# Kernel optimization log

Measured on AMD Instinct MI355X. Metric: run time of the kernel, lower is better.

Reference implementation:

```python
import jax, jax.numpy as jnp
import numpy as np

N_NODES = 30000
N_EDGES = 480000
N0, N1 = 64, 16            # hidden irreps: 64x0e (scalars) + 16x1o (vectors)
NUM_LAYERS = 3
NUM_ATOM_TYPES = 100
ATOM_EMB = 64
BOND_DIM, RAD_DIM = 8, 8   # edge_attr_dim=16 -> dim//2 bonded, (dim+1)//2 radial
MAX_RADIUS = 5.0
DEG_NORM = 1.0 / (16.0 ** 0.5)   # 1/sqrt(avg degree), NequIP-style aggregation norm


def soft_one_hot(d, number=RAD_DIM):
    # e3nn soft_one_hot_linspace, basis='gaussian', cutoff=True
    values = jnp.linspace(0.0, MAX_RADIUS, number + 2)[1:-1]
    step = MAX_RADIUS / (number + 1)
    diff = (d[:, None] - values) / step
    return jnp.exp(-diff ** 2) / 1.12


def setup_inputs() -> dict:
    key = jax.random.key(0)
    ks = jax.random.split(key, 16)
    pos = jax.random.normal(ks[0], (N_NODES, 3), jnp.float32) * 2.0
    edge_index = jax.random.randint(ks[1], (2, N_EDGES), 0, N_NODES)
    bond_mask = jax.random.randint(ks[2], (N_EDGES,), 0, 2)
    atom_type = jax.random.randint(ks[3], (N_NODES,), 0, NUM_ATOM_TYPES)

    def p(k, shape, scale):
        return jax.random.normal(k, shape, jnp.float32) * scale

    W_TP = N0 + N1 + N0 + 2 * N1   # per-edge tensor-product path weights (176)
    atom_emb = p(ks[4], (NUM_ATOM_TYPES, ATOM_EMB), 1.0)
    bond_emb = p(ks[5], (2, BOND_DIM), 1.0)
    w_init = p(ks[6], (ATOM_EMB, N0), ATOM_EMB ** -0.5)
    mlp_w1 = p(ks[7], (NUM_LAYERS, BOND_DIM + RAD_DIM, 64), 16 ** -0.5)
    mlp_b1 = jnp.zeros((NUM_LAYERS, 64), jnp.float32)
    mlp_w2 = p(ks[8], (NUM_LAYERS, 64, W_TP), 64 ** -0.5)
    lin_s = p(ks[9], (NUM_LAYERS, N0 + N1, N0), (N0 + N1) ** -0.5)
    lin_v = p(ks[10], (NUM_LAYERS, N0 + 2 * N1, N1), (N0 + 2 * N1) ** -0.5)
    gate_w = p(ks[11], (NUM_LAYERS, N0, N1), N0 ** -0.5)
    hs1 = p(ks[12], (N0, N0), N0 ** -0.5)
    hg = p(ks[13], (N0, N1), N0 ** -0.5)
    hs2 = p(ks[14], (N0, 1), N0 ** -0.5)
    hv2 = p(ks[15], (N1, 1), N1 ** -0.5)
    return dict(pos=pos, edge_index=edge_index, bond_mask=bond_mask,
                atom_type=atom_type, atom_emb=atom_emb, bond_emb=bond_emb,
                w_init=w_init, mlp_w1=mlp_w1, mlp_b1=mlp_b1, mlp_w2=mlp_w2,
                lin_s=lin_s, lin_v=lin_v, gate_w=gate_w,
                hs1=hs1, hg=hg, hs2=hs2, hv2=hv2)


def reference(pos, edge_index, bond_mask, atom_type, atom_emb, bond_emb,
              w_init, mlp_w1, mlp_b1, mlp_w2, lin_s, lin_v, gate_w,
              hs1, hg, hs2, hv2):
    n = pos.shape[0]
    src, dst = edge_index[0], edge_index[1]
    edge_vec = pos[src] - pos[dst]                       # [E,3] irregular gather
    r = jnp.linalg.norm(edge_vec, axis=-1)               # [E]
    u = edge_vec / jnp.maximum(r, 1e-9)[:, None]
    # Spherical harmonics lmax=1, 'component' normalization: Y0=1, Y1=sqrt(3)*r_hat
    y1 = (3.0 ** 0.5) * u                                # [E,3]
    edge_attr = jnp.concatenate([bond_emb[bond_mask], soft_one_hot(r)], axis=-1)  # [E,16]

    s = atom_emb[atom_type] @ w_init                     # [N,N0]; initial_linear (0e only)
    v = jnp.zeros((n, N1, 3), pos.dtype)                 # [N,N1,3]; 1o starts at zero

    for l in range(NUM_LAYERS):
        # radial/edge MLP -> per-edge tensor-product path weights
        w = jax.nn.silu(edge_attr @ mlp_w1[l] + mlp_b1[l]) @ mlp_w2[l]   # [E,176]
        w_ss, w_vs, w_sv, w_vv, w_cx = jnp.split(
            w, [N0, N0 + N1, 2 * N0 + N1, 2 * N0 + 2 * N1], axis=-1)
        se, ve = s[src], v[src]
        # CG tensor-product paths (Y0==1 absorbed):
        #   0e x 0e -> 0e (w_ss), 1o x 1o -> 0e dot (w_vs),
        #   0e x 1o -> 1o (w_sv), 1o x 0e -> 1o (w_vv), 1o x 1o -> 1e~cross (w_cx)
        m_s = jnp.concatenate(
            [w_ss * se, w_vs * jnp.einsum('eic,ec->ei', ve, y1)], axis=-1)  # [E,N0+N1]
        m_v = jnp.concatenate([
            w_sv[:, :, None] * se[:, :, None] * y1[:, None, :],
            w_vv[:, :, None] * ve,
            w_cx[:, :, None] * jnp.cross(ve, y1[:, None, :]),
        ], axis=1)                                       # [E,N0+2*N1,3]
        agg_s = jax.ops.segment_sum(m_s, dst, num_segments=n) * DEG_NORM
        agg_v = jax.ops.segment_sum(m_v, dst, num_segments=n) * DEG_NORM
        out_s = agg_s @ lin_s[l]                         # irrep-wise Linear, 0e
        out_v = jnp.einsum('nic,io->noc', agg_v, lin_v[l])  # irrep-wise Linear, 1o
        # gated nonlinearity + residual self-connection
        s = s + jax.nn.silu(out_s)
        v = v + out_v * jax.nn.sigmoid(out_s @ gate_w[l])[:, :, None]

    # EquivariantMLP output head -> 1x0e + 1x1o per node
    h = jax.nn.silu(s @ hs1)                             # [N,N0]
    vg = v * jax.nn.sigmoid(h @ hg)[:, :, None]          # gated vectors
    pred_s = h @ hs2                                     # [N,1]
    pred_v = jnp.einsum('nic,io->noc', vg, hv2)[:, 0, :] # [N,3]
    return jnp.concatenate([pred_s, pred_v], axis=-1)    # [N,4]
```

## Files before the change

kernel.cpp:

```cpp
#include <hip/hip_runtime.h>
#include <math.h>

#define N_NODES 30000
#define N_EDGES 480000
#define DEGN 0.25f
#define NBLK 1875
#define TPITCH 52

#define FENCE() do { asm volatile("" ::: "memory"); __builtin_amdgcn_sched_barrier(0); } while(0)

typedef __attribute__((ext_vector_type(8))) short short8;
typedef __attribute__((ext_vector_type(4))) float f32x4;

__device__ __forceinline__ float fsilu(float x){ return x / (1.f + __expf(-x)); }
__device__ __forceinline__ float fsig (float x){ return 1.f / (1.f + __expf(-x)); }

__device__ __forceinline__ unsigned bf16rn(float x){
  unsigned u = __float_as_uint(x);
  return (u + 0x7fffu + ((u>>16)&1u)) >> 16;
}
__device__ __forceinline__ unsigned pack2(float a, float b){
  return bf16rn(a) | (bf16rn(b)<<16);
}
__device__ __forceinline__ float bflo(unsigned u){ return __uint_as_float(u<<16); }
__device__ __forceinline__ float bfhi(unsigned u){ return __uint_as_float(u & 0xffff0000u); }

__global__ __launch_bounds__(256) void count2(const int* __restrict__ ei,
                                              int* __restrict__ deg_src,
                                              int* __restrict__ deg_dst)
{
  int e = blockIdx.x*256 + threadIdx.x;
  if (e >= N_EDGES) return;
  atomicAdd(deg_src + ei[e], 1);
  atomicAdd(deg_dst + ei[N_EDGES + e], 1);
}

__global__ __launch_bounds__(1024) void scan_deg2(
    const int* __restrict__ deg_src, int* __restrict__ off_src, int* __restrict__ cur_src,
    const int* __restrict__ deg_dst, int* __restrict__ off_dst, int* __restrict__ cur_dst)
{
  const int* deg = blockIdx.x ? deg_dst : deg_src;
  int* off = blockIdx.x ? off_dst : off_src;
  int* cur = blockIdx.x ? cur_dst : cur_src;
  __shared__ int part[1024];
  int t = threadIdx.x;
  int base = t*30;
  int local[30];
  int s = 0;
  #pragma unroll
  for (int i=0;i<30;i++){
    int idx = base + i;
    int d = (idx < N_NODES) ? deg[idx] : 0;
    local[i] = s; s += d;
  }
  part[t] = s; __syncthreads();
  for (int stp=1; stp<1024; stp<<=1){
    int v = (t >= stp) ? part[t-stp] : 0;
    __syncthreads();
    part[t] += v;
    __syncthreads();
  }
  int prefix = (t==0) ? 0 : part[t-1];
  #pragma unroll
  for (int i=0;i<30;i++){
    int idx = base + i;
    if (idx < N_NODES){ int o = prefix + local[i]; off[idx] = o; cur[idx] = o; }
  }
  if (t == 1023) off[N_NODES] = part[1023];
}

__global__ __launch_bounds__(256) void scatter_src(const int* __restrict__ ei,
                                                   int* __restrict__ cur,
                                                   int* __restrict__ csr_src,
                                                   int* __restrict__ pos_src)
{
  int e = blockIdx.x*256 + threadIdx.x;
  if (e >= N_EDGES) return;
  int p = atomicAdd(cur + ei[e], 1);
  csr_src[p] = e;
  pos_src[e] = p;
}

__global__ __launch_bounds__(256) void scatter_dst(const int* __restrict__ ei,
                                                   const int* __restrict__ pos_src,
                                                   int* __restrict__ cur,
                                                   int* __restrict__ gidx)
{
  int e = blockIdx.x*256 + threadIdx.x;
  if (e >= N_EDGES) return;
  int p = atomicAdd(cur + ei[N_EDGES + e], 1);
  gidx[p] = pos_src[e];
}

__global__ __launch_bounds__(256) void prep_edges2(
    const float* __restrict__ pos, const int* __restrict__ ei,
    const int* __restrict__ bond_mask, const float* __restrict__ bond_emb,
    const int* __restrict__ csr_src, uint4* __restrict__ rec)
{
  int k = blockIdx.x*256 + threadIdx.x;
  if (k >= N_EDGES) return;
  int e = csr_src[k];
  int src = ei[e], dst = ei[N_EDGES + e];
  float ax = pos[src*3+0], ay = pos[src*3+1], az = pos[src*3+2];
  float bx = pos[dst*3+0], by = pos[dst*3+1], bz = pos[dst*3+2];
  float vx = ax-bx, vy = ay-by, vz = az-bz;
  float r = sqrtf(vx*vx + vy*vy + vz*vz);
  float inv = 1.f / fmaxf(r, 1e-9f);
  const float s3 = 1.7320508075688772f;
  float yx = s3*vx*inv, yy = s3*vy*inv, yz = s3*vz*inv;
  int bm = bond_mask[e];
  float eav[16];
  #pragma unroll
  for (int q=0;q<8;q++) eav[q] = bond_emb[bm*8+q];
  const float step = 5.0f/9.0f;
  #pragma unroll
  for (int j=0;j<8;j++){
    float vj = (float)(j+1)*step;
    float d = (r - vj)/step;
    eav[8+j] = __expf(-d*d) * (1.0f/1.12f);
  }
  uint4 r0, r1, r2;
  r0.x = pack2(eav[0],eav[1]);  r0.y = pack2(eav[2],eav[3]);
  r0.z = pack2(eav[4],eav[5]);  r0.w = pack2(eav[6],eav[7]);
  r1.x = pack2(eav[8],eav[9]);  r1.y = pack2(eav[10],eav[11]);
  r1.z = pack2(eav[12],eav[13]);r1.w = pack2(eav[14],eav[15]);
  r2.x = __float_as_uint(yx); r2.y = __float_as_uint(yy);
  r2.z = __float_as_uint(yz); r2.w = (unsigned)src;
  rec[(size_t)k*3+0] = r0;
  rec[(size_t)k*3+1] = r1;
  rec[(size_t)k*3+2] = r2;
}

__global__ void prep_weights(const float* __restrict__ w2,
                             unsigned short* __restrict__ w2hi,
                             unsigned short* __restrict__ w2lo)
{
  int i = blockIdx.x*256 + threadIdx.x;
  if (i >= 3*176*64) return;
  int l = i / (176*64); int rem = i - l*(176*64);
  int n = rem / 64, k = rem - n*64;
  float w = w2[(size_t)l*64*176 + (size_t)k*176 + n];
  unsigned hi = bf16rn(w);
  float lo = w - __uint_as_float(hi<<16);
  w2hi[i] = (unsigned short)hi;
  w2lo[i] = (unsigned short)bf16rn(lo);
}

__global__ __launch_bounds__(256) void init_nodes(
    const int* __restrict__ atom_type, const float* __restrict__ atom_emb,
    const float* __restrict__ w_init, float* __restrict__ s)
{
  int n = blockIdx.x*256 + threadIdx.x;
  if (n >= N_NODES) return;
  int t = atom_type[n];
  float acc[64];
  #pragma unroll
  for (int o=0;o<64;o++) acc[o]=0.f;
  for (int k=0;k<64;k++){
    float ek = atom_emb[t*64+k];
    #pragma unroll
    for (int o=0;o<64;o++) acc[o] = fmaf(ek, w_init[k*64+o], acc[o]);
  }
  float4* so = (float4*)(s + (size_t)n*64);
  #pragma unroll
  for (int q=0;q<16;q++) so[q] = make_float4(acc[4*q],acc[4*q+1],acc[4*q+2],acc[4*q+3]);
}

__device__ __forceinline__ void mfma_tile(
    const unsigned short* __restrict__ W2hi, const unsigned short* __restrict__ W2lo,
    int colbase, const short8 (&bfr)[4][2], int wv, int l, unsigned char* tb)
{
  const unsigned short* ap = W2hi + (size_t)(colbase+(l&15))*64 + ((l>>4)*8);
  const unsigned short* aq = W2lo + (size_t)(colbase+(l&15))*64 + ((l>>4)*8);
  short8 ah0 = *(const short8*)ap;
  short8 ah1 = *(const short8*)(ap+32);
  short8 al0 = *(const short8*)aq;
  short8 al1 = *(const short8*)(aq+32);
  #pragma unroll
  for (int ntg=0;ntg<4;ntg++){
    f32x4 acc = {0.f,0.f,0.f,0.f};
    acc = __builtin_amdgcn_mfma_f32_16x16x32_bf16(ah0, bfr[ntg][0], acc, 0,0,0);
    acc = __builtin_amdgcn_mfma_f32_16x16x32_bf16(ah1, bfr[ntg][1], acc, 0,0,0);
    acc = __builtin_amdgcn_mfma_f32_16x16x32_bf16(al0, bfr[ntg][0], acc, 0,0,0);
    acc = __builtin_amdgcn_mfma_f32_16x16x32_bf16(al1, bfr[ntg][1], acc, 0,0,0);
    int e = wv*64 + ntg*16 + (l&15);
    uint2 pk; pk.x = pack2(acc[0],acc[1]); pk.y = pack2(acc[2],acc[3]);
    *(uint2*)(tb + (size_t)e*TPITCH + ((l>>4)*8)) = pk;
  }
}

__device__ __forceinline__ void decode_w(const unsigned char* tb, int t, float* w)
{
  const unsigned char* wr = tb + (size_t)t*TPITCH;
  uint4 c0 = *(const uint4*)wr;
  uint4 c1 = *(const uint4*)(wr+16);
  w[0]=bflo(c0.x); w[1]=bfhi(c0.x); w[2]=bflo(c0.y); w[3]=bfhi(c0.y);
  w[4]=bflo(c0.z); w[5]=bfhi(c0.z); w[6]=bflo(c0.w); w[7]=bfhi(c0.w);
  w[8]=bflo(c1.x); w[9]=bfhi(c1.x); w[10]=bflo(c1.y); w[11]=bfhi(c1.y);
  w[12]=bflo(c1.z); w[13]=bfhi(c1.z); w[14]=bflo(c1.w); w[15]=bfhi(c1.w);
}

__device__ __forceinline__ void consume_sv(const float* w, int i0,
    const float* __restrict__ ssrc, const float* __restrict__ linv, float* a_o)
{
  #pragma unroll
  for (int q4=0;q4<4;q4++){
    float4 s4 = *(const float4*)(ssrc + i0 + q4*4);
    float tq[4] = { w[q4*4+0]*s4.x, w[q4*4+1]*s4.y, w[q4*4+2]*s4.z, w[q4*4+3]*s4.w };
    #pragma unroll
    for (int qq=0;qq<4;qq++){
      int i = i0 + q4*4 + qq;
      float tv = tq[qq];
      #pragma unroll
      for (int o=0;o<16;o++) a_o[o] = fmaf(tv, linv[i*16+o], a_o[o]);
    }
  }
}

__device__ __forceinline__ void direct_wss(
    const unsigned short* __restrict__ W2hi, const unsigned short* __restrict__ W2lo,
    int colbase, const short8 (&bfr)[4][2], int wv, int l, int src,
    const float* __restrict__ s, uint4* __restrict__ msg4, int kb0)
{
  const unsigned short* ap = W2hi + (size_t)(colbase+(l&15))*64 + ((l>>4)*8);
  const unsigned short* aq = W2lo + (size_t)(colbase+(l&15))*64 + ((l>>4)*8);
  short8 ah0 = *(const short8*)ap;
  short8 ah1 = *(const short8*)(ap+32);
  short8 al0 = *(const short8*)aq;
  short8 al1 = *(const short8*)(aq+32);
  int cb = colbase + ((l>>4)<<2);
  #pragma unroll
  for (int ntg=0;ntg<4;ntg++){
    f32x4 acc = {0.f,0.f,0.f,0.f};
    acc = __builtin_amdgcn_mfma_f32_16x16x32_bf16(ah0, bfr[ntg][0], acc, 0,0,0);
    acc = __builtin_amdgcn_mfma_f32_16x16x32_bf16(ah1, bfr[ntg][1], acc, 0,0,0);
    acc = __builtin_amdgcn_mfma_f32_16x16x32_bf16(al0, bfr[ntg][0], acc, 0,0,0);
    acc = __builtin_amdgcn_mfma_f32_16x16x32_bf16(al1, bfr[ntg][1], acc, 0,0,0);
    int j2 = ntg*16 + (l&15);
    int src2 = __shfl(src, j2);
    float4 s4 = *(const float4*)(s + (size_t)src2*64 + cb);
    uint2 o2;
    o2.x = pack2(DEGN*acc[0]*s4.x, DEGN*acc[1]*s4.y);
    o2.y = pack2(DEGN*acc[2]*s4.z, DEGN*acc[3]*s4.w);
    int ke2 = kb0 + wv*64 + j2;
    unsigned* mb = (unsigned*)(msg4 + ((size_t)(ke2>>1))*32 + (cb>>3)*2 + (ke2&1));
    *(uint2*)(mb + ((cb>>2)&1)*2) = o2;
  }
}

__global__ __launch_bounds__(256)
void edge_fused2(
    const uint4* __restrict__ rec,
    const float* __restrict__ s, const float* __restrict__ v,
    const float* __restrict__ W1,
    const float* __restrict__ b1,
    const unsigned short* __restrict__ W2hi,
    const unsigned short* __restrict__ W2lo,
    const float* __restrict__ linv,
    uint4* __restrict__ msg4)
{
  __shared__ __align__(16) unsigned char lds[59392];
  int t = threadIdx.x;
  int ke = blockIdx.x*256 + t;

  uint4 r0 = rec[(size_t)ke*3+0];
  uint4 r1 = rec[(size_t)ke*3+1];
  uint4 r2 = rec[(size_t)ke*3+2];
  float yx = __uint_as_float(r2.x), yy = __uint_as_float(r2.y), yz = __uint_as_float(r2.z);
  int src = (int)r2.w;

  {
    float eav[16];
    eav[0]=bflo(r0.x); eav[1]=bfhi(r0.x); eav[2]=bflo(r0.y); eav[3]=bfhi(r0.y);
    eav[4]=bflo(r0.z); eav[5]=bfhi(r0.z); eav[6]=bflo(r0.w); eav[7]=bfhi(r0.w);
    eav[8]=bflo(r1.x); eav[9]=bfhi(r1.x); eav[10]=bflo(r1.y); eav[11]=bfhi(r1.y);
    eav[12]=bflo(r1.z); eav[13]=bfhi(r1.z); eav[14]=bflo(r1.w); eav[15]=bfhi(r1.w);
    float h[64];
    #pragma unroll
    for (int k=0;k<64;k++) h[k] = b1[k];
    #pragma unroll
    for (int j=0;j<16;j++){
      float a = eav[j];
      #pragma unroll
      for (int k=0;k<64;k++) h[k] = fmaf(a, W1[j*64+k], h[k]);
    }
    #pragma unroll
    for (int k=0;k<64;k++) h[k] = fsilu(h[k]);
    #pragma unroll
    for (int q=0;q<8;q++){
      uint4 hp;
      hp.x = pack2(h[8*q+0],h[8*q+1]); hp.y = pack2(h[8*q+2],h[8*q+3]);
      hp.z = pack2(h[8*q+4],h[8*q+5]); hp.w = pack2(h[8*q+6],h[8*q+7]);
      int byte = (t*128 + q*16) ^ ((t&7)<<4);
      *(uint4*)(lds + byte) = hp;
    }
  }
  FENCE();

  int wv = t>>6, l = t&63;
  short8 bfr[4][2];
  #pragma unroll
  for (int ntg=0;ntg<4;ntg++){
    int erow = wv*64 + ntg*16 + (l&15);
    #pragma unroll
    for (int kk=0;kk<2;kk++){
      int byte = (erow*128 + kk*64 + ((l>>4)*16)) ^ ((erow&7)<<4);
      bfr[ntg][kk] = *(const short8*)(lds + byte);
    }
  }
  FENCE();

  unsigned char* tbA = lds + 32768;
  unsigned char* tbB = lds + 46080;
  const float* ssrc = s + (size_t)src*64;
  const float4* vsrc4 = (const float4*)(v + (size_t)src*48);
  uint4* mrow = msg4 + ((size_t)(ke>>1))*32 + (ke&1);

  float a_o[16];
  #pragma unroll
  for (int o=0;o<16;o++) a_o[o]=0.f;
  #pragma unroll 1
  for (int st=0; st<2; ++st){
    mfma_tile(W2hi, W2lo, 80+st*32,    bfr, wv, l, tbA);
    mfma_tile(W2hi, W2lo, 80+st*32+16, bfr, wv, l, tbB);
    FENCE();
    float wa[16], wb[16];
    decode_w(tbA, t, wa);
    decode_w(tbB, t, wb);
    consume_sv(wa, st*32,    ssrc, linv, a_o);
    consume_sv(wb, st*32+16, ssrc, linv, a_o);
    FENCE();
  }

  mfma_tile(W2hi, W2lo, 144, bfr, wv, l, tbA);
  mfma_tile(W2hi, W2lo, 160, bfr, wv, l, tbB);
  FENCE();
  {
    float wvv[16], wcx[16];
    decode_w(tbA, t, wvv);
    decode_w(tbB, t, wcx);
    #pragma unroll 1
    for (int hf=0; hf<2; ++hf){
      int ob = hf*8;
      float av[24];
      #pragma unroll
      for (int q=0;q<24;q++) av[q]=0.f;
      #pragma unroll
      for (int j4=0;j4<4;j4++){
        float4 a = vsrc4[j4*3+0];
        float4 b = vsrc4[j4*3+1];
        float4 c = vsrc4[j4*3+2];
        float vx_[4] = {a.x, a.w, b.z, c.y};
        float vy_[4] = {a.y, b.x, b.w, c.z};
        float vz_[4] = {a.z, b.y, c.x, c.w};
        #pragma unroll
        for (int jj=0;jj<4;jj++){
          int j = j4*4+jj;
          float cxv = vy_[jj]*yz - vz_[jj]*yy;
          float cyv = vz_[jj]*yx - vx_[jj]*yz;
          float czv = vx_[jj]*yy - vy_[jj]*yx;
          float w1 = wvv[j], w2 = wcx[j];
          #pragma unroll
          for (int o=0;o<8;o++){
            float t1 = w1*linv[(64+j)*16+ob+o];
            float t2 = w2*linv[(80+j)*16+ob+o];
            av[o*3+0] = fmaf(t1, vx_[jj], fmaf(t2, cxv, av[o*3+0]));
            av[o*3+1] = fmaf(t1, vy_[jj], fmaf(t2, cyv, av[o*3+1]));
            av[o*3+2] = fmaf(t1, vz_[jj], fmaf(t2, czv, av[o*3+2]));
          }
        }
      }
      #pragma unroll
      for (int o=0;o<8;o++){
        av[o*3+0] = fmaf(a_o[ob+o], yx, av[o*3+0]);
        av[o*3+1] = fmaf(a_o[ob+o], yy, av[o*3+1]);
        av[o*3+2] = fmaf(a_o[ob+o], yz, av[o*3+2]);
      }
      #pragma unroll
      for (int b2=0;b2<3;b2++){
        uint4 p;
        p.x = pack2(DEGN*av[8*b2+0], DEGN*av[8*b2+1]);
        p.y = pack2(DEGN*av[8*b2+2], DEGN*av[8*b2+3]);
        p.z = pack2(DEGN*av[8*b2+4], DEGN*av[8*b2+5]);
        p.w = pack2(DEGN*av[8*b2+6], DEGN*av[8*b2+7]);
        mrow[(10+hf*3+b2)*2] = p;
      }
    }
  }
  FENCE();

  int kb0 = blockIdx.x*256;
  #pragma unroll 1
  for (int st=0; st<2; ++st){
    direct_wss(W2hi, W2lo, st*32,    bfr, wv, l, src, s, msg4, kb0);
    direct_wss(W2hi, W2lo, st*32+16, bfr, wv, l, src, s, msg4, kb0);
    FENCE();
  }

  {
    const unsigned short* ap = W2hi + (size_t)(64+(l&15))*64 + ((l>>4)*8);
    const unsigned short* aq = W2lo + (size_t)(64+(l&15))*64 + ((l>>4)*8);
    short8 ah0 = *(const short8*)ap;
    short8 ah1 = *(const short8*)(ap+32);
    short8 al0 = *(const short8*)aq;
    short8 al1 = *(const short8*)(aq+32);
    int jb = (l>>4)<<2;
    #pragma unroll
    for (int ntg=0;ntg<4;ntg++){
      f32x4 acc = {0.f,0.f,0.f,0.f};
      acc = __builtin_amdgcn_mfma_f32_16x16x32_bf16(ah0, bfr[ntg][0], acc, 0,0,0);
      acc = __builtin_amdgcn_mfma_f32_16x16x32_bf16(ah1, bfr[ntg][1], acc, 0,0,0);
      acc = __builtin_amdgcn_mfma_f32_16x16x32_bf16(al0, bfr[ntg][0], acc, 0,0,0);
      acc = __builtin_amdgcn_mfma_f32_16x16x32_bf16(al1, bfr[ntg][1], acc, 0,0,0);
      int j2 = ntg*16 + (l&15);
      int src2 = __shfl(src, j2);
      float eyx = __shfl(yx, j2), eyy = __shfl(yy, j2), eyz = __shfl(yz, j2);
      const float* vp = v + (size_t)src2*48 + jb*3;
      float4 va = *(const float4*)(vp);
      float4 vb = *(const float4*)(vp+4);
      float4 vc = *(const float4*)(vp+8);
      float d0 = va.x*eyx + va.y*eyy + va.z*eyz;
      float d1 = va.w*eyx + vb.x*eyy + vb.y*eyz;
      float d2 = vb.z*eyx + vb.w*eyy + vc.x*eyz;
      float d3 = vc.y*eyx + vc.z*eyy + vc.w*eyz;
      uint2 o2;
      o2.x = pack2(DEGN*acc[0]*d0, DEGN*acc[1]*d1);
      o2.y = pack2(DEGN*acc[2]*d2, DEGN*acc[3]*d3);
      int ke2 = kb0 + wv*64 + j2;
      int i64 = 64 + jb;
      unsigned* mb = (unsigned*)(msg4 + ((size_t)(ke2>>1))*32 + (i64>>3)*2 + (ke2&1));
      *(uint2*)(mb + ((i64>>2)&1)*2) = o2;
    }
  }
}

__global__ __launch_bounds__(256) void gather_nodes(
    const uint4* __restrict__ msg4,
    const int* __restrict__ off,
    const int* __restrict__ gidx,
    float* __restrict__ agg)
{
  int tid = threadIdx.x;
  int n = blockIdx.x*16 + (tid >> 4);
  int l = tid & 15;
  if (n >= N_NODES) return;
  float acc[8];
  #pragma unroll
  for (int q=0;q<8;q++) acc[q]=0.f;
  int k1 = off[n+1];
  for (int k=off[n]; k<k1; k++){
    int m = gidx[k];
    uint4 mm = msg4[((size_t)(m>>1))*32 + l*2 + (m&1)];
    acc[0] += bflo(mm.x); acc[1] += bfhi(mm.x);
    acc[2] += bflo(mm.y); acc[3] += bfhi(mm.y);
    acc[4] += bflo(mm.z); acc[5] += bfhi(mm.z);
    acc[6] += bflo(mm.w); acc[7] += bfhi(mm.w);
  }
  float4* o = (float4*)(agg + (size_t)n*128 + l*8);
  o[0] = make_float4(acc[0],acc[1],acc[2],acc[3]);
  o[1] = make_float4(acc[4],acc[5],acc[6],acc[7]);
}

__global__ __launch_bounds__(256) void node_update(
    const float* __restrict__ agg,
    const float* __restrict__ lin_s, const float* __restrict__ gate_w,
    float* __restrict__ s, float* __restrict__ v)
{
  int n = blockIdx.x*256 + threadIdx.x;
  if (n >= N_NODES) return;
  const float* row = agg + (size_t)n*128;
  float outs[64];
  #pragma unroll
  for (int o=0;o<64;o++) outs[o]=0.f;
  for (int i=0;i<80;i+=4){
    float4 a4 = *(const float4*)(row + i);
    float av[4]={a4.x,a4.y,a4.z,a4.w};
    #pragma unroll
    for (int q=0;q<4;q++){
      float a = av[q];
      #pragma unroll
      for (int o=0;o<64;o++) outs[o] = fmaf(a, lin_s[(i+q)*64+o], outs[o]);
    }
  }
  float g[16];
  #pragma unroll
  for (int j=0;j<16;j++) g[j]=0.f;
  for (int o=0;o<64;o++){
    float x = outs[o];
    #pragma unroll
    for (int j=0;j<16;j++) g[j] = fmaf(x, gate_w[o*16+j], g[j]);
    s[(size_t)n*64+o] += fsilu(x);
  }
  #pragma unroll
  for (int j=0;j<16;j++){
    float gv = fsig(g[j]);
    v[(size_t)n*48+j*3+0] += row[80+j*3+0]*gv;
    v[(size_t)n*48+j*3+1] += row[80+j*3+1]*gv;
    v[(size_t)n*48+j*3+2] += row[80+j*3+2]*gv;
  }
}

__global__ __launch_bounds__(256) void head_kernel(
    const float* __restrict__ s, const float* __restrict__ v,
    const float* __restrict__ hs1, const float* __restrict__ hg,
    const float* __restrict__ hs2, const float* __restrict__ hv2,
    float* __restrict__ out)
{
  int n = blockIdx.x*256 + threadIdx.x;
  if (n >= N_NODES) return;
  float sv[64];
  const float4* sp = (const float4*)(s + (size_t)n*64);
  #pragma unroll
  for (int q=0;q<16;q++){ float4 t=sp[q]; sv[4*q]=t.x; sv[4*q+1]=t.y; sv[4*q+2]=t.z; sv[4*q+3]=t.w; }
  float h[64];
  #pragma unroll
  for (int o=0;o<64;o++) h[o]=0.f;
  for (int k=0;k<64;k++){
    float x = sv[k];
    #pragma unroll
    for (int o=0;o<64;o++) h[o] = fmaf(x, hs1[k*64+o], h[o]);
  }
  #pragma unroll
  for (int o=0;o<64;o++) h[o] = fsilu(h[o]);
  float g[16];
  #pragma unroll
  for (int j=0;j<16;j++) g[j]=0.f;
  float ps = 0.f;
  for (int o=0;o<64;o++){
    float x = h[o];
    #pragma unroll
    for (int j=0;j<16;j++) g[j] = fmaf(x, hg[o*16+j], g[j]);
    ps = fmaf(x, hs2[o], ps);
  }
  float pvx=0.f, pvy=0.f, pvz=0.f;
  #pragma unroll
  for (int j=0;j<16;j++){
    float gv = fsig(g[j]) * hv2[j];
    pvx = fmaf(v[(size_t)n*48+j*3+0], gv, pvx);
    pvy = fmaf(v[(size_t)n*48+j*3+1], gv, pvy);
    pvz = fmaf(v[(size_t)n*48+j*3+2], gv, pvz);
  }
  *(float4*)(out + (size_t)n*4) = make_float4(ps, pvx, pvy, pvz);
}

extern "C" void kernel_launch(void* const* d_in, const int* in_sizes, int n_in,
                              void* d_out, int out_size, void* d_ws, size_t ws_size,
                              hipStream_t stream)
{
  const float* pos       = (const float*)d_in[0];
  const int*   ei        = (const int*)  d_in[1];
  const int*   bond_mask = (const int*)  d_in[2];
  const int*   atom_type = (const int*)  d_in[3];
  const float* atom_emb  = (const float*)d_in[4];
  const float* bond_emb  = (const float*)d_in[5];
  const float* w_init    = (const float*)d_in[6];
  const float* mlp_w1    = (const float*)d_in[7];
  const float* mlp_b1    = (const float*)d_in[8];
  const float* mlp_w2    = (const float*)d_in[9];
  const float* lin_s     = (const float*)d_in[10];
  const float* lin_v     = (const float*)d_in[11];
  const float* gate_w    = (const float*)d_in[12];
  const float* hs1       = (const float*)d_in[13];
  const float* hg        = (const float*)d_in[14];
  const float* hs2       = (const float*)d_in[15];
  const float* hv2       = (const float*)d_in[16];
  float* out = (float*)d_out;

  char* ws = (char*)d_ws;
  size_t off_b = 0;
  auto alloc = [&](size_t nbytes){ void* p = (void*)(ws + off_b); off_b += ((nbytes + 255)/256)*256; return p; };
  uint4*    rec     = (uint4*)   alloc((size_t)N_EDGES*48);
  uint4*    msg4    = (uint4*)   alloc((size_t)N_EDGES*256);
  float*    sbuf    = (float*)   alloc((size_t)N_NODES*64*4);
  float*    vbuf    = (float*)   alloc((size_t)N_NODES*48*4);
  float*    agg     = (float*)   alloc((size_t)N_NODES*128*4);
  unsigned short* w2hi = (unsigned short*)alloc((size_t)3*176*64*2);
  unsigned short* w2lo = (unsigned short*)alloc((size_t)3*176*64*2);
  int*      deg_src = (int*)     alloc((size_t)N_NODES*4);
  int*      deg_dst = (int*)     alloc((size_t)N_NODES*4);
  int*      off_src = (int*)     alloc((size_t)(N_NODES+1)*4);
  int*      off_dst = (int*)     alloc((size_t)(N_NODES+1)*4);
  int*      cur_src = (int*)     alloc((size_t)N_NODES*4);
  int*      cur_dst = (int*)     alloc((size_t)N_NODES*4);
  int*      csr_src = (int*)     alloc((size_t)N_EDGES*4);
  int*      pos_src = (int*)     alloc((size_t)N_EDGES*4);
  int*      gidx    = (int*)     alloc((size_t)N_EDGES*4);

  dim3 blk(256);
  int gE = (N_EDGES + 255)/256;
  int gN = (N_NODES + 255)/256;
  int gG = (N_NODES + 15)/16;

  hipMemsetAsync(vbuf, 0, (size_t)N_NODES*48*sizeof(float), stream);
  hipMemsetAsync(deg_src, 0, (size_t)2*N_NODES*sizeof(int) + 512, stream);

  count2<<<gE, blk, 0, stream>>>(ei, deg_src, deg_dst);
  scan_deg2<<<2, 1024, 0, stream>>>(deg_src, off_src, cur_src, deg_dst, off_dst, cur_dst);
  scatter_src<<<gE, blk, 0, stream>>>(ei, cur_src, csr_src, pos_src);
  scatter_dst<<<gE, blk, 0, stream>>>(ei, pos_src, cur_dst, gidx);

  prep_edges2<<<gE, blk, 0, stream>>>(pos, ei, bond_mask, bond_emb, csr_src, rec);
  prep_weights<<<(3*176*64 + 255)/256, blk, 0, stream>>>(mlp_w2, w2hi, w2lo);
  init_nodes<<<gN, blk, 0, stream>>>(atom_type, atom_emb, w_init, sbuf);

  for (int l=0;l<3;l++){
    edge_fused2<<<NBLK, blk, 0, stream>>>(rec, sbuf, vbuf,
        mlp_w1 + (size_t)l*16*64, mlp_b1 + (size_t)l*64,
        w2hi + (size_t)l*176*64, w2lo + (size_t)l*176*64,
        lin_v + (size_t)l*96*16,
        msg4);
    gather_nodes<<<gG, blk, 0, stream>>>(msg4, off_dst, gidx, agg);
    node_update<<<gN, blk, 0, stream>>>(agg,
        lin_s + (size_t)l*80*64, gate_w + (size_t)l*64*16, sbuf, vbuf);
  }
  head_kernel<<<gN, blk, 0, stream>>>(sbuf, vbuf, hs1, hg, hs2, hv2, out);
}
```

Baseline: 1.189 ms.

## Fuse node gather with node update via shared-memory row staging

Merges the per-node gather of bf16 messages with the node update into one kernel. Each 16-lane group stages its aggregated row in LDS, and each lane computes 4 of the 64 scalar outputs. The gate products are reduced across lanes with xor shuffles. This drops the fp32 agg buffer round trip and one launch, and spreads the per-node 80x64 matvec over 16 lanes instead of one thread holding 64 accumulators. The early exit for out-of-range nodes is removed, but 30000 divides evenly by 16, so every node index stays in range.

```diff
diff --git a/kernel.cpp b/kernel.cpp
--- a/kernel.cpp
+++ b/kernel.cpp
@@ -434,16 +434,20 @@
   }
 }
 
-__global__ __launch_bounds__(256) void gather_nodes(
+#define RPAD 132
+__global__ __launch_bounds__(256) void gather_update(
     const uint4* __restrict__ msg4,
     const int* __restrict__ off,
     const int* __restrict__ gidx,
-    float* __restrict__ agg)
-{
+    const float* __restrict__ lin_s, const float* __restrict__ gate_w,
+    float* __restrict__ s, float* __restrict__ v)
+{
+  __shared__ float rows[16*RPAD];
   int tid = threadIdx.x;
-  int n = blockIdx.x*16 + (tid >> 4);
+  int nl = tid >> 4;
   int l = tid & 15;
-  if (n >= N_NODES) return;
+  int n = blockIdx.x*16 + nl;
+
   float acc[8];
   #pragma unroll
   for (int q=0;q<8;q++) acc[q]=0.f;
@@ -456,48 +460,49 @@
     acc[4] += bflo(mm.z); acc[5] += bfhi(mm.z);
     acc[6] += bflo(mm.w); acc[7] += bfhi(mm.w);
   }
-  float4* o = (float4*)(agg + (size_t)n*128 + l*8);
-  o[0] = make_float4(acc[0],acc[1],acc[2],acc[3]);
-  o[1] = make_float4(acc[4],acc[5],acc[6],acc[7]);
-}
-
-__global__ __launch_bounds__(256) void node_update(
-    const float* __restrict__ agg,
-    const float* __restrict__ lin_s, const float* __restrict__ gate_w,
-    float* __restrict__ s, float* __restrict__ v)
-{
-  int n = blockIdx.x*256 + threadIdx.x;
-  if (n >= N_NODES) return;
-  const float* row = agg + (size_t)n*128;
-  float outs[64];
-  #pragma unroll
-  for (int o=0;o<64;o++) outs[o]=0.f;
-  for (int i=0;i<80;i+=4){
-    float4 a4 = *(const float4*)(row + i);
-    float av[4]={a4.x,a4.y,a4.z,a4.w};
-    #pragma unroll
-    for (int q=0;q<4;q++){
-      float a = av[q];
-      #pragma unroll
-      for (int o=0;o<64;o++) outs[o] = fmaf(a, lin_s[(i+q)*64+o], outs[o]);
-    }
+  float* row = rows + nl*RPAD;
+  *(float4*)(row + l*8)     = make_float4(acc[0],acc[1],acc[2],acc[3]);
+  *(float4*)(row + l*8 + 4) = make_float4(acc[4],acc[5],acc[6],acc[7]);
+  __syncthreads();
+
+  float o4[4] = {0.f,0.f,0.f,0.f};
+  for (int i=0;i<80;i++){
+    float a = row[i];
+    float4 w4 = *(const float4*)(lin_s + i*64 + l*4);
+    o4[0] = fmaf(a, w4.x, o4[0]);
+    o4[1] = fmaf(a, w4.y, o4[1]);
+    o4[2] = fmaf(a, w4.z, o4[2]);
+    o4[3] = fmaf(a, w4.w, o4[3]);
+  }
+  {
+    float4 sold = *(const float4*)(s + (size_t)n*64 + l*4);
+    float4 snew;
+    snew.x = sold.x + fsilu(o4[0]);
+    snew.y = sold.y + fsilu(o4[1]);
+    snew.z = sold.z + fsilu(o4[2]);
+    snew.w = sold.w + fsilu(o4[3]);
+    *(float4*)(s + (size_t)n*64 + l*4) = snew;
   }
   float g[16];
   #pragma unroll
   for (int j=0;j<16;j++) g[j]=0.f;
-  for (int o=0;o<64;o++){
-    float x = outs[o];
+  #pragma unroll
+  for (int c=0;c<4;c++){
+    float x = o4[c];
+    int o = l*4+c;
     #pragma unroll
     for (int j=0;j<16;j++) g[j] = fmaf(x, gate_w[o*16+j], g[j]);
-    s[(size_t)n*64+o] += fsilu(x);
-  }
-  #pragma unroll
-  for (int j=0;j<16;j++){
-    float gv = fsig(g[j]);
-    v[(size_t)n*48+j*3+0] += row[80+j*3+0]*gv;
-    v[(size_t)n*48+j*3+1] += row[80+j*3+1]*gv;
-    v[(size_t)n*48+j*3+2] += row[80+j*3+2]*gv;
-  }
+  }
+  #pragma unroll
+  for (int m2=1; m2<16; m2<<=1){
+    #pragma unroll
+    for (int j=0;j<16;j++) g[j] += __shfl_xor(g[j], m2);
+  }
+  float gv = fsig(g[l]);
+  float* vp = v + (size_t)n*48 + l*3;
+  vp[0] += row[80+l*3+0]*gv;
+  vp[1] += row[80+l*3+1]*gv;
+  vp[2] += row[80+l*3+2]*gv;
 }
 
 __global__ __launch_bounds__(256) void head_kernel(
@@ -573,7 +578,6 @@
   uint4*    msg4    = (uint4*)   alloc((size_t)N_EDGES*256);
   float*    sbuf    = (float*)   alloc((size_t)N_NODES*64*4);
   float*    vbuf    = (float*)   alloc((size_t)N_NODES*48*4);
-  float*    agg     = (float*)   alloc((size_t)N_NODES*128*4);
   unsigned short* w2hi = (unsigned short*)alloc((size_t)3*176*64*2);
   unsigned short* w2lo = (unsigned short*)alloc((size_t)3*176*64*2);
   int*      deg_src = (int*)     alloc((size_t)N_NODES*4);
@@ -609,8 +613,7 @@
         w2hi + (size_t)l*176*64, w2lo + (size_t)l*176*64,
         lin_v + (size_t)l*96*16,
         msg4);
-    gather_nodes<<<gG, blk, 0, stream>>>(msg4, off_dst, gidx, agg);
-    node_update<<<gN, blk, 0, stream>>>(agg,
+    gather_update<<<gG, blk, 0, stream>>>(msg4, off_dst, gidx,
         lin_s + (size_t)l*80*64, gate_w + (size_t)l*64*16, sbuf, vbuf);
   }
   head_kernel<<<gN, blk, 0, stream>>>(sbuf, vbuf, hs1, hg, hs2, hv2, out);
```

Result: faster. 1.130 ms (-5.0%).
